# Kernel optimization log

Hardware: AMD Instinct MI355X
Metric: run time of the kernel (lower is better)

## Reference

```python
import jax, jax.numpy as jnp
from jax import lax
import numpy as np

B, T, F, H = 256, 64, 256, 64  # batch, window_size, num_features, hidden (enc=dec)


def setup_inputs() -> dict:
    key = jax.random.key(0)
    ks = jax.random.split(key, 12)
    def n(k, shape, s=0.05):
        return jax.random.normal(k, shape, jnp.float32) * s
    return {
        "inputs": jax.random.normal(ks[0], (B, T, F), jnp.float32),
        # encoder LSTMCell (input = x_tilde of size F)
        "enc_kernel": n(ks[1], (F, 4 * H)),
        "enc_rec": n(ks[2], (H, 4 * H)),
        "enc_bias": jnp.zeros((4 * H,), jnp.float32),
        # decoder LSTMCell (input = y_tilde of size H)
        "dec_kernel": n(ks[3], (H, 4 * H)),
        "dec_rec": n(ks[4], (H, 4 * H)),
        "dec_bias": jnp.zeros((4 * H,), jnp.float32),
        # encoder attention: Dense(T, tanh) on [h;s;x_series] then Dense(1)
        "attn_e_W": n(ks[5], (2 * H + T, T)),
        "attn_e_b": jnp.zeros((T,), jnp.float32),
        "attn_e_v": n(ks[6], (T, 1)),
        "attn_e_vb": jnp.zeros((1,), jnp.float32),
        # decoder attention: Dense(H_enc, tanh) on [d;c;h_enc] then Dense(1)
        "attn_d_W": n(ks[7], (2 * H + H, H)),
        "attn_d_b": jnp.zeros((H,), jnp.float32),
        "attn_d_v": n(ks[8], (H, 1)),
        "attn_d_vb": jnp.zeros((1,), jnp.float32),
        # fc: (context H_enc + y_prev 1) -> H_dec
        "fc_W": n(ks[9], (H + 1, H)),
        "fc_b": jnp.zeros((H,), jnp.float32),
        # fc_final: (d_n H_dec + context H_enc) -> num_features
        "fcf_W": n(ks[10], (2 * H, F)),
        "fcf_b": jnp.zeros((F,), jnp.float32),
    }


def _lstm_step(x, h, c, K, R, b):
    # Keras LSTMCell gate order: i, f, g(candidate), o
    z = x @ K + h @ R + b
    i, f, g, o = jnp.split(z, 4, axis=-1)
    c_new = jax.nn.sigmoid(f) * c + jax.nn.sigmoid(i) * jnp.tanh(g)
    h_new = jax.nn.sigmoid(o) * jnp.tanh(c_new)
    return h_new, c_new


def _forward(inputs, enc_kernel, enc_rec, enc_bias, dec_kernel, dec_rec, dec_bias,
             attn_e_W, attn_e_b, attn_e_v, attn_e_vb,
             attn_d_W, attn_d_b, attn_d_v, attn_d_vb,
             fc_W, fc_b, fcf_W, fcf_b):
    Bn, Tn, Fn = inputs.shape
    Hn = enc_kernel.shape[1] // 4

    # ---------------- encoder (input attention over features) ----------------
    We_h, We_s, We_x = attn_e_W[:Hn], attn_e_W[Hn:2 * Hn], attn_e_W[2 * Hn:]
    x_series = jnp.transpose(inputs, (0, 2, 1))                 # (B, F, T): per-feature time series
    x_proj = jnp.einsum('bft,tu->bfu', x_series, We_x)          # (B, F, T), state-independent, hoisted

    def enc_step(carry, x_t):
        h, s = carry                                            # (B, H) each
        hs = h @ We_h + s @ We_s + attn_e_b                     # (B, T)
        e = jnp.tanh(hs[:, None, :] + x_proj)                   # (B, F, T)
        score = (e @ attn_e_v)[..., 0] + attn_e_vb              # (B, F)
        alpha = jax.nn.softmax(score, axis=1)                   # attention over features
        x_tilde = alpha * x_t                                   # (B, F)
        h2, s2 = _lstm_step(x_tilde, h, s, enc_kernel, enc_rec, enc_bias)
        return (h2, s2), h2

    z0 = jnp.zeros((Bn, Hn), inputs.dtype)
    _, h_all = lax.scan(enc_step, (z0, z0), jnp.transpose(inputs, (1, 0, 2)))
    x_encoded = jnp.transpose(h_all, (1, 0, 2))                 # (B, T, H)

    # ---------------- decoder (temporal attention over encoder states) ----------------
    Wd_d, Wd_c, Wd_x = attn_d_W[:Hn], attn_d_W[Hn:2 * Hn], attn_d_W[2 * Hn:]
    xe_proj = jnp.einsum('bte,eu->btu', x_encoded, Wd_x)        # (B, T, H), hoisted
    y_prev = inputs[:, :, -1]                                   # (B, T)

    def dec_step(carry, y_t):
        d, c = carry
        dc = d @ Wd_d + c @ Wd_c + attn_d_b                     # (B, H)
        e = jnp.tanh(dc[:, None, :] + xe_proj)                  # (B, T, H)
        score = (e @ attn_d_v)[..., 0] + attn_d_vb              # (B, T)
        beta = jax.nn.softmax(score, axis=1)                    # attention over time
        context = jnp.einsum('bt,bte->be', beta, x_encoded)     # (B, H)
        y_tilde = jnp.concatenate([context, y_t[:, None]], axis=1) @ fc_W + fc_b
        d2, c2 = _lstm_step(y_tilde, d, c, dec_kernel, dec_rec, dec_bias)
        return (d2, c2), context

    (d_n, _), ctxs = lax.scan(dec_step, (z0, z0), y_prev.T)
    context = ctxs[-1]                                          # context from last step
    y_pred = jnp.concatenate([d_n, context], axis=1) @ fcf_W + fcf_b  # (B, F)
    return y_pred[:, None, :]                                   # (B, 1, F)


def reference(inputs, enc_kernel, enc_rec, enc_bias, dec_kernel, dec_rec, dec_bias,
              attn_e_W, attn_e_b, attn_e_v, attn_e_vb,
              attn_d_W, attn_d_b, attn_d_v, attn_d_vb,
              fc_W, fc_b, fcf_W, fcf_b):
    return _forward(inputs, enc_kernel, enc_rec, enc_bias, dec_kernel, dec_rec, dec_bias,
                    attn_e_W, attn_e_b, attn_e_v, attn_e_vb,
                    attn_d_W, attn_d_b, attn_d_v, attn_d_vb,
                    fc_W, fc_b, fcf_W, fcf_b)
```

## Files before the change

### kernel.cpp

```cpp
#include <hip/hip_runtime.h>
#include <math.h>

#define ALIGN16 __attribute__((aligned(16)))

__device__ __forceinline__ float rcpf_(float x){ return __builtin_amdgcn_rcpf(x); }
__device__ __forceinline__ float tanh_e(float x){
  float t = __expf(2.0f*x);
  return (t - 1.0f) * rcpf_(t + 1.0f);
}
__device__ __forceinline__ float sigm(float x){
  return rcpf_(1.0f + __expf(-x));
}

__global__ __launch_bounds__(256, 1)
void darnn_fused(const float* __restrict__ gin,
                 const float* __restrict__ eKg,
                 const float* __restrict__ eRg,
                 const float* __restrict__ ebg,
                 const float* __restrict__ dKg,
                 const float* __restrict__ dRg,
                 const float* __restrict__ dbg,
                 const float* __restrict__ aeW,
                 const float* __restrict__ aeb,
                 const float* __restrict__ aev,
                 const float* __restrict__ adW,
                 const float* __restrict__ adb,
                 const float* __restrict__ adv,
                 const float* __restrict__ fcW,
                 const float* __restrict__ fcb,
                 const float* __restrict__ fcfW,
                 const float* __restrict__ fcfb,
                 float* __restrict__ out)
{
  __shared__ ALIGN16 float s_w[4160];
  __shared__ ALIGN16 float s_xenc[64*68];
  __shared__ ALIGN16 float s_ag[256];
  __shared__ ALIGN16 float s_xtld[256];
  __shared__ ALIGN16 float s_hs[64];
  __shared__ ALIGN16 float s_pe[64];
  __shared__ ALIGN16 float s_redB[4];
  __shared__ ALIGN16 float s_ctx[64];
  __shared__ ALIGN16 float s_yprev[64];
  __shared__ ALIGN16 float s_h[64];
  __shared__ ALIGN16 float s_c[64];
  __shared__ ALIGN16 float s_aev[64];

  const int tid  = threadIdx.x;
  const int lane = tid & 63;
  const int wv   = tid >> 6;
  const int u4   = tid >> 2;
  const int g4   = tid & 3;
  const int b    = blockIdx.x;
  const float* inb = gin + (size_t)b * (64*256);

  for (int i = tid; i < 4096; i += 256) s_w[i] = aeW[8192 + i];
  if (tid < 64) { s_aev[tid] = aev[tid]; s_h[tid] = 0.f; s_c[tid] = 0.f; }
  __syncthreads();

  float P[64];
#pragma unroll
  for (int i = 0; i < 64; ++i) P[i] = 0.f;
  for (int t = 0; t < 64; ++t) {
    float xv = inb[t*256 + tid];
#pragma unroll
    for (int q = 0; q < 16; ++q) {
      float4 w = *(const float4*)&s_w[t*64 + q*4];
      P[q*4+0] = fmaf(xv, w.x, P[q*4+0]);
      P[q*4+1] = fmaf(xv, w.y, P[q*4+1]);
      P[q*4+2] = fmaf(xv, w.z, P[q*4+2]);
      P[q*4+3] = fmaf(xv, w.w, P[q*4+3]);
    }
  }
#pragma unroll
  for (int i = 0; i < 64; ++i) P[i] = __expf(2.0f*P[i]);
  float vsum = 0.f;
#pragma unroll
  for (int q = 0; q < 16; ++q) {
    float4 v = *(const float4*)&s_aev[q*4];
    vsum += (v.x + v.y) + (v.z + v.w);
  }

  float eKr[256];
#pragma unroll
  for (int q = 0; q < 256; ++q) eKr[q] = eKg[q*256 + tid];
  float eRr[64];
#pragma unroll
  for (int j = 0; j < 64; ++j) eRr[j] = eRg[j*256 + tid];
  float wh[16], wsr[16];
#pragma unroll
  for (int jj = 0; jj < 16; ++jj) {
    wh[jj]  = aeW[(g4*16 + jj)*64 + u4];
    wsr[jj] = aeW[(64 + g4*16 + jj)*64 + u4];
  }
  const float aeb_u = aeb[u4];
  const float eb_k  = ebg[tid];

  for (int t = 0; t < 64; ++t) {
    float xtv = inb[t*256 + tid];
    float p0 = 0.f, p1 = 0.f;
#pragma unroll
    for (int q = 0; q < 4; ++q) {
      float4 h4 = *(const float4*)&s_h[g4*16 + q*4];
      float4 c4 = *(const float4*)&s_c[g4*16 + q*4];
      p0 = fmaf(h4.x, wh[q*4+0], p0);  p0 = fmaf(h4.y, wh[q*4+1], p0);
      p0 = fmaf(h4.z, wh[q*4+2], p0);  p0 = fmaf(h4.w, wh[q*4+3], p0);
      p1 = fmaf(c4.x, wsr[q*4+0], p1); p1 = fmaf(c4.y, wsr[q*4+1], p1);
      p1 = fmaf(c4.z, wsr[q*4+2], p1); p1 = fmaf(c4.w, wsr[q*4+3], p1);
    }
    float p = p0 + p1;
    p += __shfl_xor(p, 1); p += __shfl_xor(p, 2);
    float E = __expf(2.0f*(p + aeb_u));
    if (g4 == 0) s_hs[u4] = E;
    __syncthreads();

    float sA = 0.f, sB = 0.f, sC = 0.f, sD = 0.f;
#pragma unroll
    for (int q = 0; q < 16; ++q) {
      float4 Ev = *(const float4*)&s_hs[q*4];
      float4 vv = *(const float4*)&s_aev[q*4];
      sA = fmaf(vv.x, rcpf_(fmaf(Ev.x, P[q*4+0], 1.f)), sA);
      sB = fmaf(vv.y, rcpf_(fmaf(Ev.y, P[q*4+1], 1.f)), sB);
      sC = fmaf(vv.z, rcpf_(fmaf(Ev.z, P[q*4+2], 1.f)), sC);
      sD = fmaf(vv.w, rcpf_(fmaf(Ev.w, P[q*4+3], 1.f)), sD);
    }
    float sc = fmaf(-2.f, (sA+sB)+(sC+sD), vsum);
    float pe = __expf(sc);
    float ws = pe;
    ws += __shfl_xor(ws,1);  ws += __shfl_xor(ws,2);  ws += __shfl_xor(ws,4);
    ws += __shfl_xor(ws,8);  ws += __shfl_xor(ws,16); ws += __shfl_xor(ws,32);
    if (lane == 0) s_redB[wv] = ws;
    s_xtld[tid] = pe * xtv;
    __syncthreads();

    float4 r = *(const float4*)&s_redB[0];
    float invS = rcpf_((r.x + r.y) + (r.z + r.w));
    float a0 = 0.f, a1 = 0.f, a2 = 0.f, a3 = 0.f;
#pragma unroll
    for (int q = 0; q < 64; ++q) {
      float4 x4 = *(const float4*)&s_xtld[q*4];
      a0 = fmaf(x4.x, eKr[q*4+0], a0);
      a1 = fmaf(x4.y, eKr[q*4+1], a1);
      a2 = fmaf(x4.z, eKr[q*4+2], a2);
      a3 = fmaf(x4.w, eKr[q*4+3], a3);
    }
    float h0 = 0.f, h1 = 0.f;
#pragma unroll
    for (int q = 0; q < 16; ++q) {
      float4 h4 = *(const float4*)&s_h[q*4];
      h0 = fmaf(h4.x, eRr[q*4+0], h0); h1 = fmaf(h4.y, eRr[q*4+1], h1);
      h0 = fmaf(h4.z, eRr[q*4+2], h0); h1 = fmaf(h4.w, eRr[q*4+3], h1);
    }
    float v = fmaf((a0+a1)+(a2+a3), invS, (h0+h1) + eb_k);
    float a = (wv == 2) ? tanh_e(v) : sigm(v);
    s_ag[tid] = a;
    __syncthreads();

    if (tid < 64) {
      float gi = s_ag[tid], gf = s_ag[64+tid], gg = s_ag[128+tid], go = s_ag[192+tid];
      float cn = fmaf(gf, s_c[tid], gi*gg);
      float hn = go * tanh_e(cn);
      s_c[tid] = cn; s_h[tid] = hn; s_xenc[t*68 + tid] = hn;
    }
    __syncthreads();
  }

  for (int i = tid; i < 4096; i += 256) s_w[i] = adW[8192 + i];
  if (tid < 64) { s_h[tid] = 0.f; s_c[tid] = 0.f; s_yprev[tid] = inb[tid*256 + 255]; }
  __syncthreads();

  float pd_[16];
  {
    float xe[16];
#pragma unroll
    for (int i = 0; i < 16; ++i) xe[i] = 0.f;
    for (int e = 0; e < 64; ++e) {
      float xv = s_xenc[u4*68 + e];
#pragma unroll
      for (int q = 0; q < 4; ++q) {
        float4 w = *(const float4*)&s_w[e*64 + g4*16 + q*4];
        xe[q*4+0] = fmaf(xv, w.x, xe[q*4+0]);
        xe[q*4+1] = fmaf(xv, w.y, xe[q*4+1]);
        xe[q*4+2] = fmaf(xv, w.z, xe[q*4+2]);
        xe[q*4+3] = fmaf(xv, w.w, xe[q*4+3]);
      }
    }
#pragma unroll
    for (int i = 0; i < 16; ++i) pd_[i] = __expf(2.0f*xe[i]);
  }
  float dKr[64];
#pragma unroll
  for (int j = 0; j < 64; ++j) dKr[j] = dKg[j*256 + tid];
  __syncthreads();
  for (int i = tid; i < 4160; i += 256) s_w[i] = fcW[i];
  __syncthreads();

  float m2k = 0.f, mbk = dbg[tid];
  float macc[64];
#pragma unroll
  for (int e = 0; e < 64; ++e) {
    float c0 = 0.f, c1 = 0.f;
#pragma unroll
    for (int q = 0; q < 16; ++q) {
      float4 w = *(const float4*)&s_w[e*64 + q*4];
      c0 = fmaf(w.x, dKr[q*4+0], c0); c1 = fmaf(w.y, dKr[q*4+1], c1);
      c0 = fmaf(w.z, dKr[q*4+2], c0); c1 = fmaf(w.w, dKr[q*4+3], c1);
    }
    macc[e] = c0 + c1;
  }
#pragma unroll
  for (int q = 0; q < 16; ++q) {
    float4 w = *(const float4*)&s_w[4096 + q*4];
    m2k = fmaf(w.x, dKr[q*4+0], m2k); m2k = fmaf(w.y, dKr[q*4+1], m2k);
    m2k = fmaf(w.z, dKr[q*4+2], m2k); m2k = fmaf(w.w, dKr[q*4+3], m2k);
    mbk = fmaf(fcb[q*4+0], dKr[q*4+0], mbk); mbk = fmaf(fcb[q*4+1], dKr[q*4+1], mbk);
    mbk = fmaf(fcb[q*4+2], dKr[q*4+2], mbk); mbk = fmaf(fcb[q*4+3], dKr[q*4+3], mbk);
  }
  float XMr[64];
#pragma unroll
  for (int t = 0; t < 64; ++t) {
    float c0 = 0.f, c1 = 0.f;
#pragma unroll
    for (int q = 0; q < 16; ++q) {
      float4 xv = *(const float4*)&s_xenc[t*68 + q*4];
      c0 = fmaf(xv.x, macc[q*4+0], c0); c1 = fmaf(xv.y, macc[q*4+1], c1);
      c0 = fmaf(xv.z, macc[q*4+2], c0); c1 = fmaf(xv.w, macc[q*4+3], c1);
    }
    XMr[t] = c0 + c1;
  }
  float dRr[64];
#pragma unroll
  for (int j = 0; j < 64; ++j) dRr[j] = dRg[j*256 + tid];
  float wdd[16], wdc[16], advr[16];
#pragma unroll
  for (int jj = 0; jj < 16; ++jj) {
    wdd[jj]  = adW[(g4*16 + jj)*64 + u4];
    wdc[jj]  = adW[(64 + g4*16 + jj)*64 + u4];
    advr[jj] = adv[g4*16 + jj];
  }
  float vsumd = 0.f;
#pragma unroll
  for (int i = 0; i < 16; ++i) vsumd += advr[i];
  vsumd += __shfl_xor(vsumd, 1); vsumd += __shfl_xor(vsumd, 2);
  const float adb_u = adb[u4];

  for (int t = 0; t < 64; ++t) {
    float p0 = 0.f, p1 = 0.f;
#pragma unroll
    for (int q = 0; q < 4; ++q) {
      float4 h4 = *(const float4*)&s_h[g4*16 + q*4];
      float4 c4 = *(const float4*)&s_c[g4*16 + q*4];
      p0 = fmaf(h4.x, wdd[q*4+0], p0);  p0 = fmaf(h4.y, wdd[q*4+1], p0);
      p0 = fmaf(h4.z, wdd[q*4+2], p0);  p0 = fmaf(h4.w, wdd[q*4+3], p0);
      p1 = fmaf(c4.x, wdc[q*4+0], p1);  p1 = fmaf(c4.y, wdc[q*4+1], p1);
      p1 = fmaf(c4.z, wdc[q*4+2], p1);  p1 = fmaf(c4.w, wdc[q*4+3], p1);
    }
    float p = p0 + p1;
    p += __shfl_xor(p, 1); p += __shfl_xor(p, 2);
    float E = __expf(2.0f*(p + adb_u));
    if (g4 == 0) s_hs[u4] = E;
    __syncthreads();

    float sA = 0.f, sB = 0.f;
#pragma unroll
    for (int q = 0; q < 4; ++q) {
      float4 Ev = *(const float4*)&s_hs[g4*16 + q*4];
      sA = fmaf(advr[q*4+0], rcpf_(fmaf(Ev.x, pd_[q*4+0], 1.f)), sA);
      sB = fmaf(advr[q*4+1], rcpf_(fmaf(Ev.y, pd_[q*4+1], 1.f)), sB);
      sA = fmaf(advr[q*4+2], rcpf_(fmaf(Ev.z, pd_[q*4+2], 1.f)), sA);
      sB = fmaf(advr[q*4+3], rcpf_(fmaf(Ev.w, pd_[q*4+3], 1.f)), sB);
    }
    float sacc = sA + sB;
    sacc += __shfl_xor(sacc, 1); sacc += __shfl_xor(sacc, 2);
    float sc = fmaf(-2.f, sacc, vsumd);
    float pe = __expf(sc);
    if (g4 == 0) s_pe[u4] = pe;
    float ws = pe;
    ws += __shfl_xor(ws,4); ws += __shfl_xor(ws,8);
    ws += __shfl_xor(ws,16); ws += __shfl_xor(ws,32);
    if (lane == 0) s_redB[wv] = ws;
    __syncthreads();

    float4 r = *(const float4*)&s_redB[0];
    float invS = rcpf_((r.x + r.y) + (r.z + r.w));
    float q0 = 0.f, q1 = 0.f;
#pragma unroll
    for (int q = 0; q < 16; ++q) {
      float4 pv = *(const float4*)&s_pe[q*4];
      q0 = fmaf(pv.x, XMr[q*4+0], q0); q1 = fmaf(pv.y, XMr[q*4+1], q1);
      q0 = fmaf(pv.z, XMr[q*4+2], q0); q1 = fmaf(pv.w, XMr[q*4+3], q1);
    }
    float r0 = 0.f, r1 = 0.f;
#pragma unroll
    for (int q = 0; q < 16; ++q) {
      float4 h4 = *(const float4*)&s_h[q*4];
      r0 = fmaf(h4.x, dRr[q*4+0], r0); r1 = fmaf(h4.y, dRr[q*4+1], r1);
      r0 = fmaf(h4.z, dRr[q*4+2], r0); r1 = fmaf(h4.w, dRr[q*4+3], r1);
    }
    float v = fmaf(q0+q1, invS, fmaf(s_yprev[t], m2k, (r0+r1) + mbk));
    float a = (wv == 2) ? tanh_e(v) : sigm(v);
    s_ag[tid] = a;
    __syncthreads();

    if (tid < 64) {
      float gi = s_ag[tid], gf = s_ag[64+tid], gg = s_ag[128+tid], go = s_ag[192+tid];
      float cn = fmaf(gf, s_c[tid], gi*gg);
      s_c[tid] = cn;
      s_h[tid] = go * tanh_e(cn);
    }
    __syncthreads();
  }

  {
    float4 r = *(const float4*)&s_redB[0];
    float invS = rcpf_((r.x + r.y) + (r.z + r.w));
    float pc = 0.f;
#pragma unroll
    for (int q = 0; q < 16; ++q)
      pc = fmaf(s_pe[g4*16 + q], s_xenc[(g4*16 + q)*68 + u4], pc);
    pc += __shfl_xor(pc, 1); pc += __shfl_xor(pc, 2);
    if (g4 == 0) s_ctx[u4] = pc * invS;
  }
  __syncthreads();

  {
    float a0 = fcfb[tid], a1 = 0.f, a2 = 0.f, a3 = 0.f;
#pragma unroll
    for (int q = 0; q < 16; ++q) {
      float4 h4 = *(const float4*)&s_h[q*4];
      a0 = fmaf(h4.x, fcfW[(q*4+0)*256 + tid], a0);
      a1 = fmaf(h4.y, fcfW[(q*4+1)*256 + tid], a1);
      a2 = fmaf(h4.z, fcfW[(q*4+2)*256 + tid], a2);
      a3 = fmaf(h4.w, fcfW[(q*4+3)*256 + tid], a3);
      float4 c4 = *(const float4*)&s_ctx[q*4];
      a0 = fmaf(c4.x, fcfW[(64 + q*4+0)*256 + tid], a0);
      a1 = fmaf(c4.y, fcfW[(64 + q*4+1)*256 + tid], a1);
      a2 = fmaf(c4.z, fcfW[(64 + q*4+2)*256 + tid], a2);
      a3 = fmaf(c4.w, fcfW[(64 + q*4+3)*256 + tid], a3);
    }
    out[b*256 + tid] = (a0 + a1) + (a2 + a3);
  }
}

extern "C" void kernel_launch(void* const* d_in, const int* in_sizes, int n_in,
                              void* d_out, int out_size, void* d_ws, size_t ws_size,
                              hipStream_t stream) {
  const float* gin  = (const float*)d_in[0];
  const float* eK   = (const float*)d_in[1];
  const float* eR   = (const float*)d_in[2];
  const float* eb   = (const float*)d_in[3];
  const float* dK   = (const float*)d_in[4];
  const float* dR   = (const float*)d_in[5];
  const float* db   = (const float*)d_in[6];
  const float* aeW  = (const float*)d_in[7];
  const float* aeb  = (const float*)d_in[8];
  const float* aev  = (const float*)d_in[9];
  const float* adW  = (const float*)d_in[11];
  const float* adb  = (const float*)d_in[12];
  const float* adv  = (const float*)d_in[13];
  const float* fcW  = (const float*)d_in[15];
  const float* fcb  = (const float*)d_in[16];
  const float* fcfW = (const float*)d_in[17];
  const float* fcfb = (const float*)d_in[18];
  float* out = (float*)d_out;

  const int B = in_sizes[0] / (64*256);
  hipLaunchKernelGGL(darnn_fused, dim3(B), dim3(256), 0, stream,
                     gin, eK, eR, eb, dK, dR, db, aeW, aeb, aev,
                     adW, adb, adv, fcW, fcb, fcfW, fcfb, out);
}
```

Before: 553.0 us.

## Replicate LSTM cell update per wave to drop a barrier, spill attention P to LDS

New measurement: 2.087 ms. 277% more time.

```diff
diff --git a/kernel.cpp b/kernel.cpp
--- a/kernel.cpp
+++ b/kernel.cpp
@@ -33,6 +33,7 @@
                  float* __restrict__ out)
 {
   __shared__ ALIGN16 float s_w[4160];
+  __shared__ ALIGN16 float s_P[256*65];
   __shared__ ALIGN16 float s_xenc[64*68];
   __shared__ ALIGN16 float s_ag[256];
   __shared__ ALIGN16 float s_xtld[256];
@@ -42,7 +43,6 @@
   __shared__ ALIGN16 float s_ctx[64];
   __shared__ ALIGN16 float s_yprev[64];
   __shared__ ALIGN16 float s_h[64];
-  __shared__ ALIGN16 float s_c[64];
   __shared__ ALIGN16 float s_aev[64];
 
   const int tid  = threadIdx.x;
@@ -54,25 +54,27 @@
   const float* inb = gin + (size_t)b * (64*256);
 
   for (int i = tid; i < 4096; i += 256) s_w[i] = aeW[8192 + i];
-  if (tid < 64) { s_aev[tid] = aev[tid]; s_h[tid] = 0.f; s_c[tid] = 0.f; }
-  __syncthreads();
-
-  float P[64];
-#pragma unroll
-  for (int i = 0; i < 64; ++i) P[i] = 0.f;
-  for (int t = 0; t < 64; ++t) {
-    float xv = inb[t*256 + tid];
-#pragma unroll
-    for (int q = 0; q < 16; ++q) {
-      float4 w = *(const float4*)&s_w[t*64 + q*4];
-      P[q*4+0] = fmaf(xv, w.x, P[q*4+0]);
-      P[q*4+1] = fmaf(xv, w.y, P[q*4+1]);
-      P[q*4+2] = fmaf(xv, w.z, P[q*4+2]);
-      P[q*4+3] = fmaf(xv, w.w, P[q*4+3]);
-    }
-  }
-#pragma unroll
-  for (int i = 0; i < 64; ++i) P[i] = __expf(2.0f*P[i]);
+  if (tid < 64) { s_aev[tid] = aev[tid]; s_h[tid] = 0.f; }
+  __syncthreads();
+
+  {
+    float xp[64];
+#pragma unroll
+    for (int i = 0; i < 64; ++i) xp[i] = 0.f;
+    for (int t = 0; t < 64; ++t) {
+      float xv = inb[t*256 + tid];
+#pragma unroll
+      for (int q = 0; q < 16; ++q) {
+        float4 w = *(const float4*)&s_w[t*64 + q*4];
+        xp[q*4+0] = fmaf(xv, w.x, xp[q*4+0]);
+        xp[q*4+1] = fmaf(xv, w.y, xp[q*4+1]);
+        xp[q*4+2] = fmaf(xv, w.z, xp[q*4+2]);
+        xp[q*4+3] = fmaf(xv, w.w, xp[q*4+3]);
+      }
+    }
+#pragma unroll
+    for (int i = 0; i < 64; ++i) s_P[tid*65 + i] = __expf(2.0f*xp[i]);
+  }
   float vsum = 0.f;
 #pragma unroll
   for (int q = 0; q < 16; ++q) {
@@ -94,18 +96,24 @@
   }
   const float aeb_u = aeb[u4];
   const float eb_k  = ebg[tid];
+  float h_j = 0.f, c_j = 0.f;
+  __syncthreads();
 
   for (int t = 0; t < 64; ++t) {
+    if (t > 0) {
+      float gi = s_ag[lane], gf = s_ag[64+lane], gg = s_ag[128+lane], go = s_ag[192+lane];
+      c_j = fmaf(gf, c_j, gi*gg);
+      h_j = go * tanh_e(c_j);
+      if (wv == 0) { s_h[lane] = h_j; s_xenc[(t-1)*68 + lane] = h_j; }
+    }
     float xtv = inb[t*256 + tid];
     float p0 = 0.f, p1 = 0.f;
 #pragma unroll
-    for (int q = 0; q < 4; ++q) {
-      float4 h4 = *(const float4*)&s_h[g4*16 + q*4];
-      float4 c4 = *(const float4*)&s_c[g4*16 + q*4];
-      p0 = fmaf(h4.x, wh[q*4+0], p0);  p0 = fmaf(h4.y, wh[q*4+1], p0);
-      p0 = fmaf(h4.z, wh[q*4+2], p0);  p0 = fmaf(h4.w, wh[q*4+3], p0);
-      p1 = fmaf(c4.x, wsr[q*4+0], p1); p1 = fmaf(c4.y, wsr[q*4+1], p1);
-      p1 = fmaf(c4.z, wsr[q*4+2], p1); p1 = fmaf(c4.w, wsr[q*4+3], p1);
+    for (int jj = 0; jj < 16; ++jj) {
+      float hh = __shfl(h_j, g4*16 + jj);
+      float cc = __shfl(c_j, g4*16 + jj);
+      p0 = fmaf(hh, wh[jj], p0);
+      p1 = fmaf(cc, wsr[jj], p1);
     }
     float p = p0 + p1;
     p += __shfl_xor(p, 1); p += __shfl_xor(p, 2);
@@ -118,10 +126,11 @@
     for (int q = 0; q < 16; ++q) {
       float4 Ev = *(const float4*)&s_hs[q*4];
       float4 vv = *(const float4*)&s_aev[q*4];
-      sA = fmaf(vv.x, rcpf_(fmaf(Ev.x, P[q*4+0], 1.f)), sA);
-      sB = fmaf(vv.y, rcpf_(fmaf(Ev.y, P[q*4+1], 1.f)), sB);
-      sC = fmaf(vv.z, rcpf_(fmaf(Ev.z, P[q*4+2], 1.f)), sC);
-      sD = fmaf(vv.w, rcpf_(fmaf(Ev.w, P[q*4+3], 1.f)), sD);
+      float4 Pv = *(const float4*)&s_P[tid*65 + q*4];
+      sA = fmaf(vv.x, rcpf_(fmaf(Ev.x, Pv.x, 1.f)), sA);
+      sB = fmaf(vv.y, rcpf_(fmaf(Ev.y, Pv.y, 1.f)), sB);
+      sC = fmaf(vv.z, rcpf_(fmaf(Ev.z, Pv.z, 1.f)), sC);
+      sD = fmaf(vv.w, rcpf_(fmaf(Ev.w, Pv.w, 1.f)), sD);
     }
     float sc = fmaf(-2.f, (sA+sB)+(sC+sD), vsum);
     float pe = __expf(sc);
@@ -135,13 +144,38 @@
     float4 r = *(const float4*)&s_redB[0];
     float invS = rcpf_((r.x + r.y) + (r.z + r.w));
     float a0 = 0.f, a1 = 0.f, a2 = 0.f, a3 = 0.f;
-#pragma unroll
-    for (int q = 0; q < 64; ++q) {
-      float4 x4 = *(const float4*)&s_xtld[q*4];
-      a0 = fmaf(x4.x, eKr[q*4+0], a0);
-      a1 = fmaf(x4.y, eKr[q*4+1], a1);
-      a2 = fmaf(x4.z, eKr[q*4+2], a2);
-      a3 = fmaf(x4.w, eKr[q*4+3], a3);
+    {
+      float4 xa[8], xb[8];
+#pragma unroll
+      for (int i = 0; i < 8; ++i) xa[i] = *(const float4*)&s_xtld[i*4];
+#pragma unroll
+      for (int g = 0; g < 8; ++g) {
+        if ((g & 1) == 0) {
+          if (g < 7) {
+#pragma unroll
+            for (int i = 0; i < 8; ++i) xb[i] = *(const float4*)&s_xtld[(g+1)*32 + i*4];
+          }
+#pragma unroll
+          for (int i = 0; i < 8; ++i) {
+            a0 = fmaf(xa[i].x, eKr[g*32 + i*4+0], a0);
+            a1 = fmaf(xa[i].y, eKr[g*32 + i*4+1], a1);
+            a2 = fmaf(xa[i].z, eKr[g*32 + i*4+2], a2);
+            a3 = fmaf(xa[i].w, eKr[g*32 + i*4+3], a3);
+          }
+        } else {
+          if (g < 7) {
+#pragma unroll
+            for (int i = 0; i < 8; ++i) xa[i] = *(const float4*)&s_xtld[(g+1)*32 + i*4];
+          }
+#pragma unroll
+          for (int i = 0; i < 8; ++i) {
+            a0 = fmaf(xb[i].x, eKr[g*32 + i*4+0], a0);
+            a1 = fmaf(xb[i].y, eKr[g*32 + i*4+1], a1);
+            a2 = fmaf(xb[i].z, eKr[g*32 + i*4+2], a2);
+            a3 = fmaf(xb[i].w, eKr[g*32 + i*4+3], a3);
+          }
+        }
+      }
     }
     float h0 = 0.f, h1 = 0.f;
 #pragma unroll
@@ -154,18 +188,17 @@
     float a = (wv == 2) ? tanh_e(v) : sigm(v);
     s_ag[tid] = a;
     __syncthreads();
-
-    if (tid < 64) {
-      float gi = s_ag[tid], gf = s_ag[64+tid], gg = s_ag[128+tid], go = s_ag[192+tid];
-      float cn = fmaf(gf, s_c[tid], gi*gg);
-      float hn = go * tanh_e(cn);
-      s_c[tid] = cn; s_h[tid] = hn; s_xenc[t*68 + tid] = hn;
-    }
-    __syncthreads();
-  }
-
+  }
+  {
+    float gi = s_ag[lane], gf = s_ag[64+lane], gg = s_ag[128+lane], go = s_ag[192+lane];
+    c_j = fmaf(gf, c_j, gi*gg);
+    h_j = go * tanh_e(c_j);
+    if (wv == 0) s_xenc[63*68 + lane] = h_j;
+  }
+
+  h_j = 0.f; c_j = 0.f;
   for (int i = tid; i < 4096; i += 256) s_w[i] = adW[8192 + i];
-  if (tid < 64) { s_h[tid] = 0.f; s_c[tid] = 0.f; s_yprev[tid] = inb[tid*256 + 255]; }
+  if (tid < 64) { s_h[tid] = 0.f; s_yprev[tid] = inb[tid*256 + 255]; }
   __syncthreads();
 
   float pd_[16];
@@ -244,15 +277,19 @@
   const float adb_u = adb[u4];
 
   for (int t = 0; t < 64; ++t) {
+    if (t > 0) {
+      float gi = s_ag[lane], gf = s_ag[64+lane], gg = s_ag[128+lane], go = s_ag[192+lane];
+      c_j = fmaf(gf, c_j, gi*gg);
+      h_j = go * tanh_e(c_j);
+      if (wv == 0) s_h[lane] = h_j;
+    }
     float p0 = 0.f, p1 = 0.f;
 #pragma unroll
-    for (int q = 0; q < 4; ++q) {
-      float4 h4 = *(const float4*)&s_h[g4*16 + q*4];
-      float4 c4 = *(const float4*)&s_c[g4*16 + q*4];
-      p0 = fmaf(h4.x, wdd[q*4+0], p0);  p0 = fmaf(h4.y, wdd[q*4+1], p0);
-      p0 = fmaf(h4.z, wdd[q*4+2], p0);  p0 = fmaf(h4.w, wdd[q*4+3], p0);
-      p1 = fmaf(c4.x, wdc[q*4+0], p1);  p1 = fmaf(c4.y, wdc[q*4+1], p1);
-      p1 = fmaf(c4.z, wdc[q*4+2], p1);  p1 = fmaf(c4.w, wdc[q*4+3], p1);
+    for (int jj = 0; jj < 16; ++jj) {
+      float hh = __shfl(h_j, g4*16 + jj);
+      float cc = __shfl(c_j, g4*16 + jj);
+      p0 = fmaf(hh, wdd[jj], p0);
+      p1 = fmaf(cc, wdc[jj], p1);
     }
     float p = p0 + p1;
     p += __shfl_xor(p, 1); p += __shfl_xor(p, 2);
@@ -300,15 +337,14 @@
     float a = (wv == 2) ? tanh_e(v) : sigm(v);
     s_ag[tid] = a;
     __syncthreads();
-
-    if (tid < 64) {
-      float gi = s_ag[tid], gf = s_ag[64+tid], gg = s_ag[128+tid], go = s_ag[192+tid];
-      float cn = fmaf(gf, s_c[tid], gi*gg);
-      s_c[tid] = cn;
-      s_h[tid] = go * tanh_e(cn);
-    }
-    __syncthreads();
-  }
+  }
+  {
+    float gi = s_ag[lane], gf = s_ag[64+lane], gg = s_ag[128+lane], go = s_ag[192+lane];
+    c_j = fmaf(gf, c_j, gi*gg);
+    h_j = go * tanh_e(c_j);
+    if (wv == 0) s_h[lane] = h_j;
+  }
+  __syncthreads();
 
   {
     float4 r = *(const float4*)&s_redB[0];
```
